# Optimization experiments

Hardware: AMD Instinct MI355X
Metric: run time of the kernel (lower is better)

Reference implementation:

```python
import jax, jax.numpy as jnp
import numpy as np


def _bce_with_logits(x, t):
    # numerically-stable binary_cross_entropy_with_logits, reduction='none'
    return jnp.maximum(x, 0.0) - x * t + jnp.log1p(jnp.exp(-jnp.abs(x)))


def _compute_weights(targets):
    """Replicates the scipy.ndimage.label / sum_labels weighting.

    4-connected component labeling (scipy default structure) via iterative
    min-label propagation, then per-pixel component area, then
    1 / (sqrt(area) + 1) with zeros replaced by the global mean of the
    nonzero sqrt-areas.
    """
    B, H, W = targets.shape
    HW = H * W  # sentinel label for background
    fg = targets > 0
    base = jnp.arange(HW, dtype=jnp.int32).reshape(1, H, W)
    lab0 = jnp.where(fg, base, HW).astype(jnp.int32)

    def cond(state):
        return state[1]

    def body(state):
        lab, _ = state
        p = jnp.pad(lab, ((0, 0), (1, 1), (1, 1)), constant_values=HW)
        nb = jnp.minimum(jnp.minimum(p[:, :-2, 1:-1], p[:, 2:, 1:-1]),
                         jnp.minimum(p[:, 1:-1, :-2], p[:, 1:-1, 2:]))
        new = jnp.where(fg, jnp.minimum(lab, nb), HW)
        return new, jnp.any(new != lab)

    lab, _ = jax.lax.while_loop(cond, body, (lab0, jnp.array(True)))

    def per_sample_area(lab_i, fg_i):
        sizes = jax.ops.segment_sum(fg_i.ravel().astype(jnp.float32),
                                    lab_i.ravel(), num_segments=HW + 1)
        return sizes[lab_i]  # [H, W] area of each pixel's component

    area = jax.vmap(per_sample_area)(lab, fg)
    area = jnp.where(fg, area, 0.0)

    w = jnp.sqrt(area)
    nz = w > 0
    # global (whole-tensor) mean of nonzero sqrt-areas, as in the torch code
    mean_nz = jnp.sum(jnp.where(nz, w, 0.0)) / jnp.maximum(
        jnp.sum(nz.astype(jnp.float32)), 1.0)
    w_filled = jnp.where(nz, w, mean_nz)
    return 1.0 / (w_filled + 1.0)


def setup_inputs() -> dict:
    key = jax.random.key(0)
    k1, k2 = jax.random.split(key)
    B, H, W = 32, 512, 512
    inputs = jax.random.normal(k1, (B, H, W), dtype=jnp.float32)
    # sparse binary mask (subcritical density -> small blobs, like vessels)
    targets = (jax.random.uniform(k2, (B, H, W)) < 0.3).astype(jnp.float32)
    return {"inputs": inputs, "targets": targets}


def reference(inputs, targets):
    weights = _compute_weights(targets)
    bce = _bce_with_logits(inputs, targets)
    return jnp.mean(weights * bce)
```

## Files before the change

### kernel.cpp

```cpp
#include <hip/hip_runtime.h>
#include <math.h>

static constexpr int IMG_W  = 512;
static constexpr int IMG_PX = 512 * 512;
static constexpr int NIMG   = 32;
static constexpr int TILE_W = 64;
static constexpr int TILE_H = 32;
static constexpr int TPX    = IMG_W / TILE_W;
static constexpr int TPY    = IMG_W / TILE_H;
static constexpr int TILES_PER_IMG = TPX * TPY;
static constexpr int FUSED_BLOCKS  = NIMG * TILES_PER_IMG;
static constexpr int SEAM_BLOCKS   = 512;
static constexpr int MIG_BLOCKS    = 512;
static constexpr int DEF_BLOCKS    = 512;
static constexpr int PART_TOTAL    = FUSED_BLOCKS + DEF_BLOCKS;
static constexpr int LCAP    = 128;
static constexpr int SCAP    = 128;
static constexpr int FLAGBIT = 1 << 30;
static constexpr int CNTMASK = FLAGBIT - 1;
static constexpr int TPIX    = TILE_W * TILE_H;


__device__ __forceinline__ int find_root_g(const int* L, int x) {
    int p = L[x];
    while (p != x) { x = p; p = L[x]; }
    return x;
}

__device__ __forceinline__ void merge_g(int* L, int a, int b) {
    while (true) {
        a = find_root_g(L, a);
        b = find_root_g(L, b);
        if (a == b) return;
        if (a < b) { int t = a; a = b; b = t; }
        int old = atomicMin(&L[a], b);
        if (old == a) return;
        a = old;
    }
}


__device__ __forceinline__ int find_root_l(volatile int* sl, int x) {
    int p = sl[x];
    while (p != x) { x = p; p = sl[x]; }
    return p;
}

__device__ __forceinline__ void merge_l(int* sl, int a, int b) {
    while (true) {
        a = find_root_l(sl, a);
        b = find_root_l(sl, b);
        if (a == b) return;
        if (a < b) { int t = a; a = b; b = t; }
        int old = atomicMin(&sl[a], b);
        if (old == a) return;
        a = old;
    }
}

__device__ __forceinline__ void block_reduce_write(float s_fg, float s_bg,
                                                   float s_sq, float s_n,
                                                   double4* __restrict__ part,
                                                   int slot) {
    for (int o = 32; o > 0; o >>= 1) {
        s_fg += __shfl_down(s_fg, o, 64);
        s_bg += __shfl_down(s_bg, o, 64);
        s_sq += __shfl_down(s_sq, o, 64);
        s_n  += __shfl_down(s_n,  o, 64);
    }
    __shared__ double4 wsum[4];
    int wave = threadIdx.x >> 6;
    if ((threadIdx.x & 63) == 0)
        wsum[wave] = make_double4((double)s_fg, (double)s_bg, (double)s_sq, (double)s_n);
    __syncthreads();
    if (threadIdx.x == 0) {
        double4 b = wsum[0];
        for (int wv = 1; wv < 4; wv++) {
            b.x += wsum[wv].x; b.y += wsum[wv].y;
            b.z += wsum[wv].z; b.w += wsum[wv].w;
        }
        part[slot] = b;
    }
}

__device__ __forceinline__ float bce0_fast(float xx) {
    return fmaxf(xx, 0.f) + __logf(1.f + __expf(-fabsf(xx)));
}


__global__ __launch_bounds__(256) void ccl_fused(const float* __restrict__ t,
                                                 const float* __restrict__ x,
                                                 int* __restrict__ L,
                                                 int* __restrict__ area,
                                                 int4* __restrict__ list,
                                                 int* __restrict__ blockcount,
                                                 int2* __restrict__ seams,
                                                 int* __restrict__ seamcount,
                                                 double4* __restrict__ part,
                                                 int* __restrict__ done) {
    __shared__ int   sl[TPIX];
    __shared__ int   cnt[TPIX];
    __shared__ float fsum[TPIX];
    __shared__ unsigned long long rowmask[TILE_H];
    __shared__ int   lcount, scount;

    int blk = blockIdx.x;
    int b   = blk / TILES_PER_IMG;
    int tid = blk % TILES_PER_IMG;
    int tY  = tid / TPX, tX = tid % TPX;
    int k   = threadIdx.x;
    int col = k & 63, wv = k >> 6;
    int base = b * IMG_PX + (tY * TILE_H) * IMG_W + tX * TILE_W;

    if (k == 0) { lcount = 0; scount = 0; }
    if (blk == 0 && k == 0) *done = 0;

    float xr[8];
#pragma unroll
    for (int s = 0; s < 8; s++) {
        int row = wv * 8 + s;
        int jj  = row * TILE_W + col;
        int g   = base + row * IMG_W + col;
        float tv = t[g];
        xr[s] = x[g];
        bool fg = (tv != 0.f);
        unsigned long long mask = __ballot(fg);
        if (col == 0) rowmask[row] = mask;
        int lab = -1;
        if (fg) {
            unsigned long long startm = mask & ~(mask << 1);
            unsigned long long low = (col == 63) ? ~0ULL : ((1ULL << (col + 1)) - 1ULL);
            lab = row * TILE_W + (63 - __clzll(startm & low));
        }
        sl[jj]   = lab;
        cnt[jj]  = 0;
        fsum[jj] = 0.f;
    }
    __syncthreads();

#pragma unroll
    for (int s = 0; s < 8; s++) {
        int row = wv * 8 + s;
        if (row == 0) continue;
        unsigned long long both = rowmask[row] & rowmask[row - 1];
        unsigned long long pairstart = both & ~(both << 1);
        if ((pairstart >> col) & 1ULL)
            merge_l(sl, row * TILE_W + col, (row - 1) * TILE_W + col);
    }
    __syncthreads();

#pragma unroll
    for (int s = 0; s < 8; s++) {
        int row = wv * 8 + s;
        unsigned long long mask = rowmask[row];
        unsigned long long startm = mask & ~(mask << 1);
        if ((startm >> col) & 1ULL) {
            unsigned long long inv = ~(mask >> col);
            int len = inv ? (__ffsll((long long)inv) - 1) : (64 - col);
            int jj = row * TILE_W + col;
            int r = find_root_l(sl, jj);
            sl[jj] = r;
            atomicAdd(&cnt[r], len);
        }
    }
    __syncthreads();

    {
        int r = -1, c = 0, dg = 0; bool owner = false;
        if      (k < 64)  { r = 0;          c = k;        dg = (tY > 0)       ? -IMG_W : 0; }
        else if (k < 128) { r = TILE_H - 1; c = k - 64;   dg = (tY < TPY - 1) ?  IMG_W : 0; owner = true; }
        else if (k < 160) { r = k - 128;    c = 0;        dg = (tX > 0)       ? -1     : 0; }
        else if (k < 192) { r = k - 160;    c = TILE_W-1; dg = (tX < TPX - 1) ?  1     : 0; owner = true; }
        if (r >= 0) {
            int jj = r * TILE_W + c;
            int s0 = sl[jj];
            if (s0 >= 0) {
                int root = sl[s0];
                int g = base + r * IMG_W + c;
                L[g] = base + (root >> 6) * IMG_W + (root & 63);
                if (dg != 0 && t[g + dg] != 0.f) {
                    atomicOr(&cnt[root], FLAGBIT);
                    if (owner) {
                        int s = atomicAdd(&scount, 1);
                        if (s < SCAP) seams[blk * SCAP + s] = make_int2(g, g + dg);
                    }
                }
            }
        }
    }
    __syncthreads();

    float s_fg = 0.f, s_bg = 0.f, s_sq = 0.f, s_n = 0.f;
#pragma unroll
    for (int s = 0; s < 8; s++) {
        int row = wv * 8 + s;
        int jj  = row * TILE_W + col;
        float xx = xr[s];
        float b0 = bce0_fast(xx);
        int s0 = sl[jj];
        if (s0 < 0) {
            s_bg += b0;
        } else {
            int root = sl[s0];
            int cc = cnt[root];
            float bce1 = b0 - xx;
            if (cc & FLAGBIT) {
                atomicAdd(&fsum[root], bce1);
            } else {
                float w = sqrtf((float)cc);
                s_fg += bce1 / (w + 1.f);
                s_sq += w;
                s_n  += 1.f;
            }
        }
    }
    __syncthreads();

    int4* mylist = list + blk * LCAP;
#pragma unroll
    for (int s = 0; s < 8; s++) {
        int jj = (wv * 8 + s) * TILE_W + col;
        if (sl[jj] == jj && (cnt[jj] & FLAGBIT)) {
            int slot = atomicAdd(&lcount, 1);
            int g = base + (jj >> 6) * IMG_W + (jj & 63);
            int c = cnt[jj] & CNTMASK;
            if (slot < LCAP)
                mylist[slot] = make_int4(g, __float_as_int(fsum[jj]), c, 0);
            area[g] = c;
            L[g]    = g;
        }
    }
    block_reduce_write(s_fg, s_bg, s_sq, s_n, part, blk);
    if (k == 0) { blockcount[blk] = min(lcount, LCAP); seamcount[blk] = min(scount, SCAP); }
}

__global__ __launch_bounds__(256) void seam_merge(int* __restrict__ L,
                                                  const int2* __restrict__ seams,
                                                  const int* __restrict__ seamcount) {
    const int nSlots = FUSED_BLOCKS * SCAP;
    int stride = gridDim.x * blockDim.x;
    for (int i = blockIdx.x * blockDim.x + threadIdx.x; i < nSlots; i += stride) {
        int blk  = i >> 7;
        int slot = i & (SCAP - 1);
        if (slot < seamcount[blk]) {
            int2 p = seams[i];
            merge_g(L, p.x, p.y);
        }
    }
}

__global__ __launch_bounds__(256) void fix_migrate(int* __restrict__ L,
                                                   int* __restrict__ area,
                                                   const int4* __restrict__ list,
                                                   const int* __restrict__ blockcount) {
    const int nSlots = FUSED_BLOCKS * LCAP;
    int stride = gridDim.x * blockDim.x;
    for (int i = blockIdx.x * blockDim.x + threadIdx.x; i < nSlots; i += stride) {
        int blk  = i >> 7;
        int slot = i & (LCAP - 1);
        if (slot < blockcount[blk]) {
            int4 ent = list[i];
            int g = ent.x;
            int r = find_root_g(L, g);
            if (r != g) { atomicAdd(&area[r], ent.z); L[g] = r; }
        }
    }
}

__global__ __launch_bounds__(256) void deferred_final(const int4* __restrict__ list,
                                                      const int* __restrict__ blockcount,
                                                      const int* __restrict__ L,
                                                      const int* __restrict__ area,
                                                      double4* __restrict__ part,
                                                      int* __restrict__ done,
                                                      float* __restrict__ out,
                                                      int N) {
    const int nSlots = FUSED_BLOCKS * LCAP;
    float s_fg = 0.f, s_sq = 0.f, s_n = 0.f;
    int stride = gridDim.x * blockDim.x;
    for (int i = blockIdx.x * blockDim.x + threadIdx.x; i < nSlots; i += stride) {
        int blk  = i >> 7;
        int slot = i & (LCAP - 1);
        if (slot < blockcount[blk]) {
            int4 ent = list[i];
            int r = find_root_g(L, ent.x);
            float w = sqrtf((float)area[r]);
            float c = (float)ent.z;
            s_fg += __int_as_float(ent.y) / (w + 1.f);
            s_sq += c * w;
            s_n  += c;
        }
    }
    block_reduce_write(s_fg, 0.f, s_sq, s_n, part, FUSED_BLOCKS + blockIdx.x);

    __shared__ int amlast;
    if (threadIdx.x == 0) {
        __threadfence();
        int old = atomicAdd(done, 1);
        amlast = (old == (int)gridDim.x - 1);
    }
    __syncthreads();
    if (!amlast) return;
    __threadfence();

    double fg = 0.0, bg = 0.0, sq = 0.0, nn = 0.0;
    for (int i = threadIdx.x; i < PART_TOTAL; i += blockDim.x) {
        double4 p = part[i];
        fg += p.x; bg += p.y; sq += p.z; nn += p.w;
    }
    for (int o = 32; o > 0; o >>= 1) {
        fg += __shfl_down(fg, o, 64);
        bg += __shfl_down(bg, o, 64);
        sq += __shfl_down(sq, o, 64);
        nn += __shfl_down(nn, o, 64);
    }
    __shared__ double4 f2[4];
    int wave = threadIdx.x >> 6;
    if ((threadIdx.x & 63) == 0) f2[wave] = make_double4(fg, bg, sq, nn);
    __syncthreads();
    if (threadIdx.x == 0) {
        double4 bb = f2[0];
        for (int wv = 1; wv < 4; wv++) {
            bb.x += f2[wv].x; bb.y += f2[wv].y;
            bb.z += f2[wv].z; bb.w += f2[wv].w;
        }
        double mean_nz = bb.z / fmax(bb.w, 1.0);
        double loss = (bb.x + bb.y / (mean_nz + 1.0)) / (double)N;
        out[0] = (float)loss;
    }
}


extern "C" void kernel_launch(void* const* d_in, const int* in_sizes, int n_in,
                              void* d_out, int out_size, void* d_ws, size_t ws_size,
                              hipStream_t stream) {
    const float* x = (const float*)d_in[0];
    const float* t = (const float*)d_in[1];
    float* out = (float*)d_out;
    int N = in_sizes[0];

    int* L          = (int*)d_ws;
    int* area       = L + N;
    double4* part   = (double4*)(area + N);
    int* blockcount = (int*)(part + PART_TOTAL);
    int* seamcount  = blockcount + FUSED_BLOCKS;
    int* done       = seamcount + FUSED_BLOCKS;
    int4* list      = (int4*)(done + 4);
    int2* seams     = (int2*)(list + FUSED_BLOCKS * LCAP);

    ccl_fused<<<FUSED_BLOCKS, 256, 0, stream>>>(t, x, L, area, list, blockcount,
                                                seams, seamcount, part, done);
    seam_merge<<<SEAM_BLOCKS, 256, 0, stream>>>(L, seams, seamcount);
    fix_migrate<<<MIG_BLOCKS, 256, 0, stream>>>(L, area, list, blockcount);
    deferred_final<<<DEF_BLOCKS, 256, 0, stream>>>(list, blockcount, L, area,
                                                   part, done, out, N);
}
```

Measured before the change: 177.5 us.

## Merge seam, migrate and final kernels into one persistent tail kernel with grid barriers

Replaces the three post-labeling kernels with a single 512-block kernel that separates its phases with software grid barriers (atomic counters plus spinning), which removes two kernel launch gaps. It also makes background pixels self-labeled so the accumulation loop is branch-free, using a per-thread foreground bitmask, and writes L=-1 for background border pixels. The spin barriers assume all 512 blocks are resident at the same time, and they add atomic traffic and spin latency.

```diff
diff --git a/kernel.cpp b/kernel.cpp
--- a/kernel.cpp
+++ b/kernel.cpp
@@ -10,10 +10,8 @@
 static constexpr int TPY    = IMG_W / TILE_H;
 static constexpr int TILES_PER_IMG = TPX * TPY;
 static constexpr int FUSED_BLOCKS  = NIMG * TILES_PER_IMG;
-static constexpr int SEAM_BLOCKS   = 512;
-static constexpr int MIG_BLOCKS    = 512;
-static constexpr int DEF_BLOCKS    = 512;
-static constexpr int PART_TOTAL    = FUSED_BLOCKS + DEF_BLOCKS;
+static constexpr int TAIL_BLOCKS   = 512;
+static constexpr int PART_TOTAL    = FUSED_BLOCKS + TAIL_BLOCKS;
 static constexpr int LCAP    = 128;
 static constexpr int SCAP    = 128;
 static constexpr int FLAGBIT = 1 << 30;
@@ -87,6 +85,18 @@
     return fmaxf(xx, 0.f) + __logf(1.f + __expf(-fabsf(xx)));
 }
 
+__device__ __forceinline__ void grid_bar(int* bar, int nblk) {
+    __syncthreads();
+    __threadfence();
+    if (threadIdx.x == 0) {
+        __hip_atomic_fetch_add(bar, 1, __ATOMIC_ACQ_REL, __HIP_MEMORY_SCOPE_AGENT);
+        while (__hip_atomic_load(bar, __ATOMIC_ACQUIRE, __HIP_MEMORY_SCOPE_AGENT) < nblk)
+            __builtin_amdgcn_s_sleep(8);
+    }
+    __syncthreads();
+    __threadfence();
+}
+
 
 __global__ __launch_bounds__(256) void ccl_fused(const float* __restrict__ t,
                                                  const float* __restrict__ x,
@@ -97,7 +107,7 @@
                                                  int2* __restrict__ seams,
                                                  int* __restrict__ seamcount,
                                                  double4* __restrict__ part,
-                                                 int* __restrict__ done) {
+                                                 int* __restrict__ bar) {
     __shared__ int   sl[TPIX];
     __shared__ int   cnt[TPIX];
     __shared__ float fsum[TPIX];
@@ -113,9 +123,10 @@
     int base = b * IMG_PX + (tY * TILE_H) * IMG_W + tX * TILE_W;
 
     if (k == 0) { lcount = 0; scount = 0; }
-    if (blk == 0 && k == 0) *done = 0;
+    if (blk == 0 && k < 4) bar[k] = 0;
 
     float xr[8];
+    unsigned int fgbits = 0;
 #pragma unroll
     for (int s = 0; s < 8; s++) {
         int row = wv * 8 + s;
@@ -124,9 +135,10 @@
         float tv = t[g];
         xr[s] = x[g];
         bool fg = (tv != 0.f);
+        fgbits |= (unsigned)fg << s;
         unsigned long long mask = __ballot(fg);
         if (col == 0) rowmask[row] = mask;
-        int lab = -1;
+        int lab = jj;
         if (fg) {
             unsigned long long startm = mask & ~(mask << 1);
             unsigned long long low = (col == 63) ? ~0ULL : ((1ULL << (col + 1)) - 1ULL);
@@ -172,11 +184,11 @@
         else if (k < 160) { r = k - 128;    c = 0;        dg = (tX > 0)       ? -1     : 0; }
         else if (k < 192) { r = k - 160;    c = TILE_W-1; dg = (tX < TPX - 1) ?  1     : 0; owner = true; }
         if (r >= 0) {
-            int jj = r * TILE_W + c;
-            int s0 = sl[jj];
-            if (s0 >= 0) {
-                int root = sl[s0];
-                int g = base + r * IMG_W + c;
+            int g = base + r * IMG_W + c;
+            bool fg = (rowmask[r] >> c) & 1ULL;
+            if (fg) {
+                int jj = r * TILE_W + c;
+                int root = sl[sl[jj]];
                 L[g] = base + (root >> 6) * IMG_W + (root & 63);
                 if (dg != 0 && t[g + dg] != 0.f) {
                     atomicOr(&cnt[root], FLAGBIT);
@@ -185,6 +197,8 @@
                         if (s < SCAP) seams[blk * SCAP + s] = make_int2(g, g + dg);
                     }
                 }
+            } else {
+                L[g] = -1;
             }
         }
     }
@@ -197,21 +211,20 @@
         int jj  = row * TILE_W + col;
         float xx = xr[s];
         float b0 = bce0_fast(xx);
-        int s0 = sl[jj];
-        if (s0 < 0) {
-            s_bg += b0;
+        int s0   = sl[jj];
+        int root = sl[s0];
+        int cc   = cnt[root];
+        bool fg  = (fgbits >> s) & 1u;
+        float bce1 = b0 - xx;
+        if (cc & FLAGBIT) {
+            atomicAdd(&fsum[root], bce1);
         } else {
-            int root = sl[s0];
-            int cc = cnt[root];
-            float bce1 = b0 - xx;
-            if (cc & FLAGBIT) {
-                atomicAdd(&fsum[root], bce1);
-            } else {
-                float w = sqrtf((float)cc);
-                s_fg += bce1 / (w + 1.f);
-                s_sq += w;
-                s_n  += 1.f;
-            }
+            float w   = sqrtf((float)cc);
+            float inv = 1.f / (w + 1.f);
+            s_fg += fg ? bce1 * inv : 0.f;
+            s_bg += fg ? 0.f : b0;
+            s_sq += w;
+            s_n  += fg ? 1.f : 0.f;
         }
     }
     __syncthreads();
@@ -234,12 +247,21 @@
     if (k == 0) { blockcount[blk] = min(lcount, LCAP); seamcount[blk] = min(scount, SCAP); }
 }
 
-__global__ __launch_bounds__(256) void seam_merge(int* __restrict__ L,
-                                                  const int2* __restrict__ seams,
-                                                  const int* __restrict__ seamcount) {
-    const int nSlots = FUSED_BLOCKS * SCAP;
-    int stride = gridDim.x * blockDim.x;
-    for (int i = blockIdx.x * blockDim.x + threadIdx.x; i < nSlots; i += stride) {
+__global__ __launch_bounds__(256) void tail(int* __restrict__ L,
+                                            int* __restrict__ area,
+                                            const int4* __restrict__ list,
+                                            const int* __restrict__ blockcount,
+                                            const int2* __restrict__ seams,
+                                            const int* __restrict__ seamcount,
+                                            double4* __restrict__ part,
+                                            int* __restrict__ bar,
+                                            float* __restrict__ out,
+                                            int N) {
+    int gtid = blockIdx.x * blockDim.x + threadIdx.x;
+    int gstride = gridDim.x * blockDim.x;
+
+    const int nS = FUSED_BLOCKS * SCAP;
+    for (int i = gtid; i < nS; i += gstride) {
         int blk  = i >> 7;
         int slot = i & (SCAP - 1);
         if (slot < seamcount[blk]) {
@@ -247,15 +269,10 @@
             merge_g(L, p.x, p.y);
         }
     }
-}
-
-__global__ __launch_bounds__(256) void fix_migrate(int* __restrict__ L,
-                                                   int* __restrict__ area,
-                                                   const int4* __restrict__ list,
-                                                   const int* __restrict__ blockcount) {
-    const int nSlots = FUSED_BLOCKS * LCAP;
-    int stride = gridDim.x * blockDim.x;
-    for (int i = blockIdx.x * blockDim.x + threadIdx.x; i < nSlots; i += stride) {
+    grid_bar(&bar[0], TAIL_BLOCKS);
+
+    const int nL = FUSED_BLOCKS * LCAP;
+    for (int i = gtid; i < nL; i += gstride) {
         int blk  = i >> 7;
         int slot = i & (LCAP - 1);
         if (slot < blockcount[blk]) {
@@ -265,20 +282,10 @@
             if (r != g) { atomicAdd(&area[r], ent.z); L[g] = r; }
         }
     }
-}
-
-__global__ __launch_bounds__(256) void deferred_final(const int4* __restrict__ list,
-                                                      const int* __restrict__ blockcount,
-                                                      const int* __restrict__ L,
-                                                      const int* __restrict__ area,
-                                                      double4* __restrict__ part,
-                                                      int* __restrict__ done,
-                                                      float* __restrict__ out,
-                                                      int N) {
-    const int nSlots = FUSED_BLOCKS * LCAP;
+    grid_bar(&bar[1], TAIL_BLOCKS);
+
     float s_fg = 0.f, s_sq = 0.f, s_n = 0.f;
-    int stride = gridDim.x * blockDim.x;
-    for (int i = blockIdx.x * blockDim.x + threadIdx.x; i < nSlots; i += stride) {
+    for (int i = gtid; i < nL; i += gstride) {
         int blk  = i >> 7;
         int slot = i & (LCAP - 1);
         if (slot < blockcount[blk]) {
@@ -292,17 +299,9 @@
         }
     }
     block_reduce_write(s_fg, 0.f, s_sq, s_n, part, FUSED_BLOCKS + blockIdx.x);
-
-    __shared__ int amlast;
-    if (threadIdx.x == 0) {
-        __threadfence();
-        int old = atomicAdd(done, 1);
-        amlast = (old == (int)gridDim.x - 1);
-    }
-    __syncthreads();
-    if (!amlast) return;
-    __threadfence();
-
+    grid_bar(&bar[2], TAIL_BLOCKS);
+
+    if (blockIdx.x != 0) return;
     double fg = 0.0, bg = 0.0, sq = 0.0, nn = 0.0;
     for (int i = threadIdx.x; i < PART_TOTAL; i += blockDim.x) {
         double4 p = part[i];
@@ -344,14 +343,12 @@
     double4* part   = (double4*)(area + N);
     int* blockcount = (int*)(part + PART_TOTAL);
     int* seamcount  = blockcount + FUSED_BLOCKS;
-    int* done       = seamcount + FUSED_BLOCKS;
-    int4* list      = (int4*)(done + 4);
+    int* bar        = seamcount + FUSED_BLOCKS;
+    int4* list      = (int4*)(bar + 4);
     int2* seams     = (int2*)(list + FUSED_BLOCKS * LCAP);
 
     ccl_fused<<<FUSED_BLOCKS, 256, 0, stream>>>(t, x, L, area, list, blockcount,
-                                                seams, seamcount, part, done);
-    seam_merge<<<SEAM_BLOCKS, 256, 0, stream>>>(L, seams, seamcount);
-    fix_migrate<<<MIG_BLOCKS, 256, 0, stream>>>(L, area, list, blockcount);
-    deferred_final<<<DEF_BLOCKS, 256, 0, stream>>>(list, blockcount, L, area,
-                                                   part, done, out, N);
-}
+                                                seams, seamcount, part, bar);
+    tail<<<TAIL_BLOCKS, 256, 0, stream>>>(L, area, list, blockcount,
+                                          seams, seamcount, part, bar, out, N);
+}
```

New measurement: 445.6 us. +151.1%, slower.
